# Kernel tuning notes

Hardware: AMD Instinct MI355X
Metric: run time of the kernel (lower is better)

Reference implementation:

```python
import jax, jax.numpy as jnp
import numpy as np

N_NODES = 100000
N_EDGES = 1600000
IN_FEATS = 64
OUT_FEATS = 16
NUM_HEADS = 4
EDGE_DIM = 5
NEG_SLOPE = 0.2


def setup_inputs() -> dict:
    key = jax.random.key(0)
    ks = jax.random.split(key, 16)
    H, D, Ed, Fi = NUM_HEADS, OUT_FEATS, EDGE_DIM, IN_FEATS
    inp = {
        "feat": jax.random.normal(ks[0], (N_NODES, Fi), jnp.float32),
        "edge_fea": jax.random.normal(ks[1], (N_EDGES, Ed), jnp.float32),
        "src": jax.random.randint(ks[2], (N_EDGES,), 0, N_NODES, jnp.int32),
        "dst": jax.random.randint(ks[3], (N_EDGES,), 0, N_NODES, jnp.int32),
        # params (xavier-ish scaling)
        "W_fc": jax.random.normal(ks[4], (Fi, H * D), jnp.float32) * (2.0 / np.sqrt(Fi + H * D)),
        "W_edg": jax.random.normal(ks[5], (Ed, H * Ed), jnp.float32) * (2.0 / np.sqrt(Ed + H * Ed)),
        "b_edg": jnp.zeros((H * Ed,), jnp.float32),
        "attn_l": jax.random.normal(ks[6], (H, D), jnp.float32) * 0.1,
        "attn_r": jax.random.normal(ks[7], (H, D), jnp.float32) * 0.1,
        "attn_edg": jax.random.normal(ks[8], (H, Ed), jnp.float32) * 0.1,
        "W_out": jax.random.normal(ks[9], (Ed + D, D), jnp.float32) * (2.0 / np.sqrt(Ed + 2 * D)),
        "b_out": jnp.zeros((D,), jnp.float32),
        "bias": jnp.zeros((H * D,), jnp.float32),
    }
    return inp


def reference(feat, edge_fea, src, dst, W_fc, W_edg, b_edg,
              attn_l, attn_r, attn_edg, W_out, b_out, bias):
    N = feat.shape[0]
    H, D = attn_l.shape
    Ed = attn_edg.shape[1]

    # node / edge projections
    feat_p = (feat @ W_fc).reshape(N, H, D)                 # [N,H,D]
    edge_p = (edge_fea @ W_edg + b_edg).reshape(-1, H, Ed)  # [E,H,Ed]

    # per-head attention logits
    el = jnp.einsum('nhd,hd->nh', feat_p, attn_l)           # [N,H]
    er = jnp.einsum('nhd,hd->nh', feat_p, attn_r)           # [N,H]
    ee = jnp.einsum('ehd,hd->eh', edge_p, attn_edg)         # [E,H]
    e = el[src] + er[dst] + ee                              # u_add_v + edge term
    e = jnp.where(e > 0, e, NEG_SLOPE * e)                  # leaky relu

    # edge softmax grouped by destination node
    m = jax.ops.segment_max(e, dst, num_segments=N)         # [N,H]
    a = jnp.exp(e - m[dst])
    z = jax.ops.segment_sum(a, dst, num_segments=N)
    a = a / z[dst]                                          # [E,H]

    # two scatter-aggregate passes
    ft_f = jax.ops.segment_sum(a[:, :, None] * edge_p, dst, num_segments=N)        # [N,H,Ed]
    ft = jax.ops.segment_sum(a[:, :, None] * feat_p[src], dst, num_segments=N)     # [N,H,D]

    rst = jnp.concatenate([ft_f, ft], axis=-1) @ W_out + b_out  # [N,H,D]
    rst = rst + bias.reshape(1, H, D)
    return rst
```

## Files before the change

kernel.cpp:

```cpp
#include <hip/hip_runtime.h>
#include <hip/hip_bf16.h>
#include <math.h>

#define NHEADS 4
#define DOUT 16
#define EDIM 5
#define CAP 128

__global__ __launch_bounds__(256) void node_proj_kernel(
    const float* __restrict__ feat, const float* __restrict__ W_fc,
    const float* __restrict__ attn_l, const float* __restrict__ attn_r,
    float* __restrict__ feat_p, float* __restrict__ el_er, int N) {
  __shared__ float wfc[64 * 64];
  for (int i = threadIdx.x; i < 64 * 64; i += 256) wfc[i] = W_fc[i];
  __syncthreads();
  const int wid  = threadIdx.x >> 6;
  const int lane = threadIdx.x & 63;
  const int n = blockIdx.x * 4 + wid;
  if (n >= N) return;

  const float f = feat[(size_t)n * 64 + lane];
  float acc = 0.f;
#pragma unroll
  for (int k = 0; k < 64; ++k) {
    const float fk = __shfl(f, k);
    acc += fk * wfc[k * 64 + lane];
  }
  feat_p[(size_t)n * 64 + lane] = acc;

  float al = acc * attn_l[lane];
  float ar = acc * attn_r[lane];
#pragma unroll
  for (int off = 1; off < 16; off <<= 1) {
    al += __shfl_xor(al, off);
    ar += __shfl_xor(ar, off);
  }
  if ((lane & 15) == 0) {
    const int h = lane >> 4;
    el_er[(size_t)n * 8 + h]     = al;
    el_er[(size_t)n * 8 + 4 + h] = ar;
  }
}

__global__ __launch_bounds__(256) void edge_logits_hist_kernel(
    const float* __restrict__ edge_fea, const int* __restrict__ src,
    const int* __restrict__ dst, const float* __restrict__ el_er,
    const float* __restrict__ W_edg, const float* __restrict__ b_edg,
    const float* __restrict__ attn_edg, float* __restrict__ e_logits,
    int* __restrict__ deg, int* __restrict__ rank, int E) {
  const int e = blockIdx.x * blockDim.x + threadIdx.x;
  if (e >= E) return;
  const int s = src[e];
  const int d = dst[e];
  rank[e] = atomicAdd(&deg[d], 1);

  float ef[5];
#pragma unroll
  for (int k = 0; k < 5; ++k) ef[k] = edge_fea[(size_t)e * 5 + k];

  const float4 elv = *(const float4*)(el_er + (size_t)s * 8);
  const float4 erv = *(const float4*)(el_er + (size_t)d * 8 + 4);
  const float elh[4] = {elv.x, elv.y, elv.z, elv.w};
  const float erh[4] = {erv.x, erv.y, erv.z, erv.w};

  float out[4];
#pragma unroll
  for (int h = 0; h < 4; ++h) {
    float ee = 0.f;
#pragma unroll
    for (int ed = 0; ed < 5; ++ed) {
      float ep = b_edg[h * 5 + ed];
#pragma unroll
      for (int k = 0; k < 5; ++k) ep += ef[k] * W_edg[k * 20 + h * 5 + ed];
      ee += ep * attn_edg[h * 5 + ed];
    }
    const float lg = elh[h] + erh[h] + ee;
    out[h] = (lg > 0.f) ? lg : 0.2f * lg;
  }
  *(float4*)(e_logits + (size_t)e * 4) = make_float4(out[0], out[1], out[2], out[3]);
}

__global__ __launch_bounds__(256) void scan_reduce_kernel(
    const int* __restrict__ deg, int* __restrict__ partial, int N) {
  const int base = blockIdx.x * 1024;
  int sum = 0;
  for (int i = threadIdx.x; i < 1024; i += 256) {
    const int idx = base + i;
    sum += (idx < N) ? deg[idx] : 0;
  }
#pragma unroll
  for (int off = 32; off >= 1; off >>= 1) sum += __shfl_xor(sum, off);
  __shared__ int ws[4];
  if ((threadIdx.x & 63) == 0) ws[threadIdx.x >> 6] = sum;
  __syncthreads();
  if (threadIdx.x == 0) partial[blockIdx.x] = ws[0] + ws[1] + ws[2] + ws[3];
}

__global__ __launch_bounds__(256) void scan_partials_kernel(
    int* __restrict__ partial, int nb) {
  __shared__ int buf[256];
  __shared__ int carry_s;
  const int t = threadIdx.x;
  if (t == 0) carry_s = 0;
  __syncthreads();
  for (int base = 0; base < nb; base += 256) {
    const int i = base + t;
    const int v = (i < nb) ? partial[i] : 0;
    buf[t] = v;
    __syncthreads();
    for (int off = 1; off < 256; off <<= 1) {
      const int tmp = (t >= off) ? buf[t - off] : 0;
      __syncthreads();
      buf[t] += tmp;
      __syncthreads();
    }
    const int carry = carry_s;
    if (i < nb) partial[i] = carry + buf[t] - v;
    __syncthreads();
    if (t == 255) carry_s = carry + buf[255];
    __syncthreads();
  }
}

__global__ __launch_bounds__(256) void scan_final_kernel(
    const int* __restrict__ deg, const int* __restrict__ partial,
    int* __restrict__ row_off, int N, int E) {
  const int b = blockIdx.x;
  const int t = threadIdx.x;
  const int lane = t & 63;
  const int wid = t >> 6;
  const int base = b * 1024 + t * 4;
  int v[4];
#pragma unroll
  for (int q = 0; q < 4; ++q) {
    const int idx = base + q;
    v[q] = (idx < N) ? deg[idx] : 0;
  }
  const int tsum = v[0] + v[1] + v[2] + v[3];
  int x = tsum;
#pragma unroll
  for (int off = 1; off < 64; off <<= 1) {
    const int tt = __shfl_up(x, off);
    if (lane >= off) x += tt;
  }
  __shared__ int ws[4];
  if (lane == 63) ws[wid] = x;
  __syncthreads();
  int wbase = 0;
  for (int w = 0; w < wid; ++w) wbase += ws[w];
  int run = partial[b] + wbase + (x - tsum);
#pragma unroll
  for (int q = 0; q < 4; ++q) {
    const int idx = base + q;
    if (idx < N) row_off[idx] = run;
    run += v[q];
  }
  if (b == 0 && t == 0) row_off[N] = E;
}

__global__ __launch_bounds__(256) void scatter_kernel(
    const int* __restrict__ dst, const int* __restrict__ row_off,
    const int* __restrict__ rank, int* __restrict__ perm, int E) {
  const int e = blockIdx.x * blockDim.x + threadIdx.x;
  if (e >= E) return;
  perm[row_off[dst[e]] + rank[e]] = e;
}

__global__ __launch_bounds__(256) void aggregate_kernel(
    const float* __restrict__ feat_p, const float* __restrict__ e_logits,
    const float* __restrict__ edge_fea, const int* __restrict__ src,
    const int* __restrict__ row_off, const int* __restrict__ perm,
    const float* __restrict__ W_edg, const float* __restrict__ b_edg,
    const float* __restrict__ W_out, const float* __restrict__ b_out,
    const float* __restrict__ bias, float* __restrict__ out, int N) {
  __shared__ float p_lds[4][CAP * 4];
  __shared__ int   s_lds[4][CAP];
  __shared__ float ef_lds[4][5 * CAP];

  const int wave = threadIdx.x >> 6;
  const int lane = threadIdx.x & 63;
  const int n = blockIdx.x * 4 + wave;
  if (n >= N) return;
  const int h = lane >> 4;
  const int d = lane & 15;

  float wcol[5];
  float be = 0.f;
  if (d < 5) {
    be = b_edg[h * 5 + d];
#pragma unroll
    for (int k = 0; k < 5; ++k) wcol[k] = W_edg[k * 20 + h * 5 + d];
  }

  const int beg = row_off[n];
  const int end = row_off[n + 1];
  const int deg = end - beg;

  float ft = 0.f, ftf = 0.f;

  if (deg <= CAP) {
    float4 mx = make_float4(-INFINITY, -INFINITY, -INFINITY, -INFINITY);
    for (int j0 = 0; j0 < deg; j0 += 64) {
      const int j = j0 + lane;
      if (j < deg) {
        const int e = perm[beg + j];
        const float4 lg = *(const float4*)(e_logits + (size_t)e * 4);
        s_lds[wave][j] = src[e];
        *(float4*)&p_lds[wave][j * 4] = lg;
#pragma unroll
        for (int k = 0; k < 5; ++k)
          ef_lds[wave][k * CAP + j] = edge_fea[(size_t)e * 5 + k];
        mx.x = fmaxf(mx.x, lg.x);
        mx.y = fmaxf(mx.y, lg.y);
        mx.z = fmaxf(mx.z, lg.z);
        mx.w = fmaxf(mx.w, lg.w);
      }
    }
#pragma unroll
    for (int off = 32; off >= 1; off >>= 1) {
      mx.x = fmaxf(mx.x, __shfl_xor(mx.x, off));
      mx.y = fmaxf(mx.y, __shfl_xor(mx.y, off));
      mx.z = fmaxf(mx.z, __shfl_xor(mx.z, off));
      mx.w = fmaxf(mx.w, __shfl_xor(mx.w, off));
    }

    float4 z = make_float4(0.f, 0.f, 0.f, 0.f);
    float4 wef[5];
#pragma unroll
    for (int k = 0; k < 5; ++k) wef[k] = make_float4(0.f, 0.f, 0.f, 0.f);
    for (int j0 = 0; j0 < deg; j0 += 64) {
      const int j = j0 + lane;
      if (j < deg) {
        const float4 lg = *(const float4*)&p_lds[wave][j * 4];
        float4 p;
        p.x = __expf(lg.x - mx.x);
        p.y = __expf(lg.y - mx.y);
        p.z = __expf(lg.z - mx.z);
        p.w = __expf(lg.w - mx.w);
        *(float4*)&p_lds[wave][j * 4] = p;
        z.x += p.x; z.y += p.y; z.z += p.z; z.w += p.w;
#pragma unroll
        for (int k = 0; k < 5; ++k) {
          const float efk = ef_lds[wave][k * CAP + j];
          wef[k].x += p.x * efk;
          wef[k].y += p.y * efk;
          wef[k].z += p.z * efk;
          wef[k].w += p.w * efk;
        }
      }
    }
#pragma unroll
    for (int off = 32; off >= 1; off >>= 1) {
      z.x += __shfl_xor(z.x, off);
      z.y += __shfl_xor(z.y, off);
      z.z += __shfl_xor(z.z, off);
      z.w += __shfl_xor(z.w, off);
#pragma unroll
      for (int k = 0; k < 5; ++k) {
        wef[k].x += __shfl_xor(wef[k].x, off);
        wef[k].y += __shfl_xor(wef[k].y, off);
        wef[k].z += __shfl_xor(wef[k].z, off);
        wef[k].w += __shfl_xor(wef[k].w, off);
      }
    }

    int j = 0;
    for (; j + 4 <= deg; j += 4) {
      const float p0 = p_lds[wave][(j + 0) * 4 + h];
      const float p1 = p_lds[wave][(j + 1) * 4 + h];
      const float p2 = p_lds[wave][(j + 2) * 4 + h];
      const float p3 = p_lds[wave][(j + 3) * 4 + h];
      const int s0 = s_lds[wave][j + 0];
      const int s1 = s_lds[wave][j + 1];
      const int s2 = s_lds[wave][j + 2];
      const int s3 = s_lds[wave][j + 3];
      const float f0 = feat_p[(size_t)s0 * 64 + lane];
      const float f1 = feat_p[(size_t)s1 * 64 + lane];
      const float f2 = feat_p[(size_t)s2 * 64 + lane];
      const float f3 = feat_p[(size_t)s3 * 64 + lane];
      ft += p0 * f0 + p1 * f1 + p2 * f2 + p3 * f3;
    }
    for (; j < deg; ++j) {
      const float p = p_lds[wave][j * 4 + h];
      const int s = s_lds[wave][j];
      ft += p * feat_p[(size_t)s * 64 + lane];
    }

    const float zh = (h == 0) ? z.x : (h == 1) ? z.y : (h == 2) ? z.z : z.w;
    const float inv = (zh > 0.f) ? 1.f / zh : 0.f;
    ft *= inv;
    if (d < 5) {
      float acc = 0.f;
#pragma unroll
      for (int k = 0; k < 5; ++k) {
        const float wk = (h == 0) ? wef[k].x : (h == 1) ? wef[k].y
                        : (h == 2) ? wef[k].z : wef[k].w;
        acc += wk * wcol[k];
      }
      ftf = acc * inv + ((zh > 0.f) ? be : 0.f);
    }
  } else {
    float mx0 = -INFINITY, mx1 = -INFINITY, mx2 = -INFINITY, mx3 = -INFINITY;
    for (int i = beg + lane; i < end; i += 64) {
      const int e = perm[i];
      const float4 lg = *(const float4*)(e_logits + (size_t)e * 4);
      mx0 = fmaxf(mx0, lg.x);
      mx1 = fmaxf(mx1, lg.y);
      mx2 = fmaxf(mx2, lg.z);
      mx3 = fmaxf(mx3, lg.w);
    }
#pragma unroll
    for (int off = 32; off >= 1; off >>= 1) {
      mx0 = fmaxf(mx0, __shfl_xor(mx0, off));
      mx1 = fmaxf(mx1, __shfl_xor(mx1, off));
      mx2 = fmaxf(mx2, __shfl_xor(mx2, off));
      mx3 = fmaxf(mx3, __shfl_xor(mx3, off));
    }
    const float mh = (h == 0) ? mx0 : (h == 1) ? mx1 : (h == 2) ? mx2 : mx3;
    float z = 0.f;
    for (int i = beg; i < end; ++i) {
      const int e = perm[i];
      const int s = src[e];
      const float lg = e_logits[(size_t)e * 4 + h];
      const float p = __expf(lg - mh);
      z += p;
      ft += p * feat_p[(size_t)s * 64 + lane];
      if (d < 5) {
        float ep = be;
#pragma unroll
        for (int k = 0; k < 5; ++k) ep += edge_fea[(size_t)e * 5 + k] * wcol[k];
        ftf += p * ep;
      }
    }
    const float inv = (z > 0.f) ? 1.f / z : 0.f;
    ft *= inv;
    ftf *= inv;
  }

  float acc = b_out[d] + bias[lane];
#pragma unroll
  for (int k = 0; k < 5; ++k)
    acc += __shfl(ftf, h * 16 + k) * W_out[k * 16 + d];
#pragma unroll
  for (int k = 0; k < 16; ++k)
    acc += __shfl(ft, h * 16 + k) * W_out[(5 + k) * 16 + d];

  out[(size_t)n * 64 + lane] = acc;
}

extern "C" void kernel_launch(void* const* d_in, const int* in_sizes, int n_in,
                              void* d_out, int out_size, void* d_ws, size_t ws_size,
                              hipStream_t stream) {
  const float* feat     = (const float*)d_in[0];
  const float* edge_fea = (const float*)d_in[1];
  const int*   src      = (const int*)d_in[2];
  const int*   dst      = (const int*)d_in[3];
  const float* W_fc     = (const float*)d_in[4];
  const float* W_edg    = (const float*)d_in[5];
  const float* b_edg    = (const float*)d_in[6];
  const float* attn_l   = (const float*)d_in[7];
  const float* attn_r   = (const float*)d_in[8];
  const float* attn_edg = (const float*)d_in[9];
  const float* W_out    = (const float*)d_in[10];
  const float* b_out    = (const float*)d_in[11];
  const float* bias     = (const float*)d_in[12];

  const int N = in_sizes[0] / 64;
  const int E = in_sizes[2];
  float* out = (float*)d_out;

  char* ws = (char*)d_ws;
  size_t off = 0;
  auto alloc = [&](size_t bytes) -> void* {
    void* p = ws + off;
    off = (off + bytes + 255) & ~(size_t)255;
    return p;
  };
  float* feat_p   = (float*)alloc((size_t)N * 64 * 4);
  float* el_er    = (float*)alloc((size_t)N * 8 * 4);
  float* e_logits = (float*)alloc((size_t)E * 4 * 4);
  int*   deg      = (int*)alloc((size_t)N * 4);
  int*   rank     = (int*)alloc((size_t)E * 4);
  int*   row_off  = (int*)alloc((size_t)(N + 1) * 4);
  int*   perm     = (int*)alloc((size_t)E * 4);
  int*   partial  = (int*)alloc((size_t)1024 * 4);
  (void)ws_size; (void)n_in; (void)out_size;

  hipMemsetAsync(deg, 0, (size_t)N * 4, stream);

  const int nblk_nodes = (N + 3) / 4;
  const int nblk_edges = (E + 255) / 256;
  const int nb_scan = (N + 1023) / 1024;

  node_proj_kernel<<<nblk_nodes, 256, 0, stream>>>(feat, W_fc, attn_l, attn_r,
                                                   feat_p, el_er, N);
  edge_logits_hist_kernel<<<nblk_edges, 256, 0, stream>>>(
      edge_fea, src, dst, el_er, W_edg, b_edg, attn_edg, e_logits, deg, rank, E);
  scan_reduce_kernel<<<nb_scan, 256, 0, stream>>>(deg, partial, N);
  scan_partials_kernel<<<1, 256, 0, stream>>>(partial, nb_scan);
  scan_final_kernel<<<nb_scan, 256, 0, stream>>>(deg, partial, row_off, N, E);
  scatter_kernel<<<nblk_edges, 256, 0, stream>>>(dst, row_off, rank, perm, E);
  aggregate_kernel<<<nblk_nodes, 256, 0, stream>>>(
      feat_p, e_logits, edge_fea, src, row_off, perm, W_edg, b_edg, W_out,
      b_out, bias, out, N);
}
```

Baseline: 536.0 us.

## Fuse edge-logit computation into aggregation and scatter edge data into CSR order

```diff
diff --git a/kernel.cpp b/kernel.cpp
--- a/kernel.cpp
+++ b/kernel.cpp
@@ -42,42 +42,12 @@
   }
 }
 
-__global__ __launch_bounds__(256) void edge_logits_hist_kernel(
-    const float* __restrict__ edge_fea, const int* __restrict__ src,
-    const int* __restrict__ dst, const float* __restrict__ el_er,
-    const float* __restrict__ W_edg, const float* __restrict__ b_edg,
-    const float* __restrict__ attn_edg, float* __restrict__ e_logits,
-    int* __restrict__ deg, int* __restrict__ rank, int E) {
+__global__ __launch_bounds__(256) void rank_kernel(
+    const int* __restrict__ dst, int* __restrict__ deg,
+    int* __restrict__ rank, int E) {
   const int e = blockIdx.x * blockDim.x + threadIdx.x;
   if (e >= E) return;
-  const int s = src[e];
-  const int d = dst[e];
-  rank[e] = atomicAdd(&deg[d], 1);
-
-  float ef[5];
-#pragma unroll
-  for (int k = 0; k < 5; ++k) ef[k] = edge_fea[(size_t)e * 5 + k];
-
-  const float4 elv = *(const float4*)(el_er + (size_t)s * 8);
-  const float4 erv = *(const float4*)(el_er + (size_t)d * 8 + 4);
-  const float elh[4] = {elv.x, elv.y, elv.z, elv.w};
-  const float erh[4] = {erv.x, erv.y, erv.z, erv.w};
-
-  float out[4];
-#pragma unroll
-  for (int h = 0; h < 4; ++h) {
-    float ee = 0.f;
-#pragma unroll
-    for (int ed = 0; ed < 5; ++ed) {
-      float ep = b_edg[h * 5 + ed];
-#pragma unroll
-      for (int k = 0; k < 5; ++k) ep += ef[k] * W_edg[k * 20 + h * 5 + ed];
-      ee += ep * attn_edg[h * 5 + ed];
-    }
-    const float lg = elh[h] + erh[h] + ee;
-    out[h] = (lg > 0.f) ? lg : 0.2f * lg;
-  }
-  *(float4*)(e_logits + (size_t)e * 4) = make_float4(out[0], out[1], out[2], out[3]);
+  rank[e] = atomicAdd(&deg[dst[e]], 1);
 }
 
 __global__ __launch_bounds__(256) void scan_reduce_kernel(
@@ -159,23 +129,29 @@
 }
 
 __global__ __launch_bounds__(256) void scatter_kernel(
-    const int* __restrict__ dst, const int* __restrict__ row_off,
-    const int* __restrict__ rank, int* __restrict__ perm, int E) {
+    const int* __restrict__ dst, const int* __restrict__ src,
+    const float* __restrict__ edge_fea, const int* __restrict__ row_off,
+    const int* __restrict__ rank, int* __restrict__ src_csr,
+    float* __restrict__ ef_csr, int E) {
   const int e = blockIdx.x * blockDim.x + threadIdx.x;
   if (e >= E) return;
-  perm[row_off[dst[e]] + rank[e]] = e;
+  const int pos = row_off[dst[e]] + rank[e];
+  src_csr[pos] = src[e];
+#pragma unroll
+  for (int k = 0; k < 5; ++k)
+    ef_csr[(size_t)pos * 5 + k] = edge_fea[(size_t)e * 5 + k];
 }
 
 __global__ __launch_bounds__(256) void aggregate_kernel(
-    const float* __restrict__ feat_p, const float* __restrict__ e_logits,
-    const float* __restrict__ edge_fea, const int* __restrict__ src,
-    const int* __restrict__ row_off, const int* __restrict__ perm,
+    const float* __restrict__ feat_p, const float* __restrict__ el_er,
+    const int* __restrict__ src_csr, const float* __restrict__ ef_csr,
+    const int* __restrict__ row_off,
     const float* __restrict__ W_edg, const float* __restrict__ b_edg,
+    const float* __restrict__ attn_edg,
     const float* __restrict__ W_out, const float* __restrict__ b_out,
     const float* __restrict__ bias, float* __restrict__ out, int N) {
   __shared__ float p_lds[4][CAP * 4];
   __shared__ int   s_lds[4][CAP];
-  __shared__ float ef_lds[4][5 * CAP];
 
   const int wave = threadIdx.x >> 6;
   const int lane = threadIdx.x & 63;
@@ -184,6 +160,24 @@
   const int h = lane >> 4;
   const int d = lane & 15;
 
+  float g[5][4];
+  float c0[4];
+#pragma unroll
+  for (int hh = 0; hh < 4; ++hh) {
+    float c = 0.f;
+#pragma unroll
+    for (int ed = 0; ed < 5; ++ed) c += b_edg[hh * 5 + ed] * attn_edg[hh * 5 + ed];
+    c0[hh] = c;
+#pragma unroll
+    for (int k = 0; k < 5; ++k) {
+      float s = 0.f;
+#pragma unroll
+      for (int ed = 0; ed < 5; ++ed)
+        s += W_edg[k * 20 + hh * 5 + ed] * attn_edg[hh * 5 + ed];
+      g[k][hh] = s;
+    }
+  }
+
   float wcol[5];
   float be = 0.f;
   if (d < 5) {
@@ -192,6 +186,7 @@
     for (int k = 0; k < 5; ++k) wcol[k] = W_edg[k * 20 + h * 5 + d];
   }
 
+  const float4 er4 = *(const float4*)(el_er + (size_t)n * 8 + 4);
   const int beg = row_off[n];
   const int end = row_off[n + 1];
   const int deg = end - beg;
@@ -199,31 +194,6 @@
   float ft = 0.f, ftf = 0.f;
 
   if (deg <= CAP) {
-    float4 mx = make_float4(-INFINITY, -INFINITY, -INFINITY, -INFINITY);
-    for (int j0 = 0; j0 < deg; j0 += 64) {
-      const int j = j0 + lane;
-      if (j < deg) {
-        const int e = perm[beg + j];
-        const float4 lg = *(const float4*)(e_logits + (size_t)e * 4);
-        s_lds[wave][j] = src[e];
-        *(float4*)&p_lds[wave][j * 4] = lg;
-#pragma unroll
-        for (int k = 0; k < 5; ++k)
-          ef_lds[wave][k * CAP + j] = edge_fea[(size_t)e * 5 + k];
-        mx.x = fmaxf(mx.x, lg.x);
-        mx.y = fmaxf(mx.y, lg.y);
-        mx.z = fmaxf(mx.z, lg.z);
-        mx.w = fmaxf(mx.w, lg.w);
-      }
-    }
-#pragma unroll
-    for (int off = 32; off >= 1; off >>= 1) {
-      mx.x = fmaxf(mx.x, __shfl_xor(mx.x, off));
-      mx.y = fmaxf(mx.y, __shfl_xor(mx.y, off));
-      mx.z = fmaxf(mx.z, __shfl_xor(mx.z, off));
-      mx.w = fmaxf(mx.w, __shfl_xor(mx.w, off));
-    }
-
     float4 z = make_float4(0.f, 0.f, 0.f, 0.f);
     float4 wef[5];
 #pragma unroll
@@ -231,21 +201,33 @@
     for (int j0 = 0; j0 < deg; j0 += 64) {
       const int j = j0 + lane;
       if (j < deg) {
-        const float4 lg = *(const float4*)&p_lds[wave][j * 4];
+        const int i = beg + j;
+        const int s = src_csr[i];
+        float ef[5];
+#pragma unroll
+        for (int k = 0; k < 5; ++k) ef[k] = ef_csr[(size_t)i * 5 + k];
+        const float4 el4 = *(const float4*)(el_er + (size_t)s * 8);
+        float lgh[4] = {el4.x + er4.x + c0[0], el4.y + er4.y + c0[1],
+                        el4.z + er4.z + c0[2], el4.w + er4.w + c0[3]};
+#pragma unroll
+        for (int k = 0; k < 5; ++k) {
+#pragma unroll
+          for (int hh = 0; hh < 4; ++hh) lgh[hh] += ef[k] * g[k][hh];
+        }
         float4 p;
-        p.x = __expf(lg.x - mx.x);
-        p.y = __expf(lg.y - mx.y);
-        p.z = __expf(lg.z - mx.z);
-        p.w = __expf(lg.w - mx.w);
+        p.x = __expf(lgh[0] > 0.f ? lgh[0] : 0.2f * lgh[0]);
+        p.y = __expf(lgh[1] > 0.f ? lgh[1] : 0.2f * lgh[1]);
+        p.z = __expf(lgh[2] > 0.f ? lgh[2] : 0.2f * lgh[2]);
+        p.w = __expf(lgh[3] > 0.f ? lgh[3] : 0.2f * lgh[3]);
+        s_lds[wave][j] = s;
         *(float4*)&p_lds[wave][j * 4] = p;
         z.x += p.x; z.y += p.y; z.z += p.z; z.w += p.w;
 #pragma unroll
         for (int k = 0; k < 5; ++k) {
-          const float efk = ef_lds[wave][k * CAP + j];
-          wef[k].x += p.x * efk;
-          wef[k].y += p.y * efk;
-          wef[k].z += p.z * efk;
-          wef[k].w += p.w * efk;
+          wef[k].x += p.x * ef[k];
+          wef[k].y += p.y * ef[k];
+          wef[k].z += p.z * ef[k];
+          wef[k].w += p.w * ef[k];
         }
       }
     }
@@ -300,41 +282,31 @@
       ftf = acc * inv + ((zh > 0.f) ? be : 0.f);
     }
   } else {
-    float mx0 = -INFINITY, mx1 = -INFINITY, mx2 = -INFINITY, mx3 = -INFINITY;
-    for (int i = beg + lane; i < end; i += 64) {
-      const int e = perm[i];
-      const float4 lg = *(const float4*)(e_logits + (size_t)e * 4);
-      mx0 = fmaxf(mx0, lg.x);
-      mx1 = fmaxf(mx1, lg.y);
-      mx2 = fmaxf(mx2, lg.z);
-      mx3 = fmaxf(mx3, lg.w);
-    }
-#pragma unroll
-    for (int off = 32; off >= 1; off >>= 1) {
-      mx0 = fmaxf(mx0, __shfl_xor(mx0, off));
-      mx1 = fmaxf(mx1, __shfl_xor(mx1, off));
-      mx2 = fmaxf(mx2, __shfl_xor(mx2, off));
-      mx3 = fmaxf(mx3, __shfl_xor(mx3, off));
-    }
-    const float mh = (h == 0) ? mx0 : (h == 1) ? mx1 : (h == 2) ? mx2 : mx3;
     float z = 0.f;
+    float wefh[5] = {0.f, 0.f, 0.f, 0.f, 0.f};
+    const float erh = (h == 0) ? er4.x : (h == 1) ? er4.y : (h == 2) ? er4.z : er4.w;
     for (int i = beg; i < end; ++i) {
-      const int e = perm[i];
-      const int s = src[e];
-      const float lg = e_logits[(size_t)e * 4 + h];
-      const float p = __expf(lg - mh);
+      const int s = src_csr[i];
+      float ef[5];
+#pragma unroll
+      for (int k = 0; k < 5; ++k) ef[k] = ef_csr[(size_t)i * 5 + k];
+      float lg = el_er[(size_t)s * 8 + h] + erh + c0[h];
+#pragma unroll
+      for (int k = 0; k < 5; ++k) lg += ef[k] * g[k][h];
+      const float p = __expf(lg > 0.f ? lg : 0.2f * lg);
       z += p;
       ft += p * feat_p[(size_t)s * 64 + lane];
-      if (d < 5) {
-        float ep = be;
-#pragma unroll
-        for (int k = 0; k < 5; ++k) ep += edge_fea[(size_t)e * 5 + k] * wcol[k];
-        ftf += p * ep;
-      }
+#pragma unroll
+      for (int k = 0; k < 5; ++k) wefh[k] += p * ef[k];
     }
     const float inv = (z > 0.f) ? 1.f / z : 0.f;
     ft *= inv;
-    ftf *= inv;
+    if (d < 5) {
+      float acc = 0.f;
+#pragma unroll
+      for (int k = 0; k < 5; ++k) acc += wefh[k] * wcol[k];
+      ftf = acc * inv + ((z > 0.f) ? be : 0.f);
+    }
   }
 
   float acc = b_out[d] + bias[lane];
@@ -376,14 +348,14 @@
     off = (off + bytes + 255) & ~(size_t)255;
     return p;
   };
-  float* feat_p   = (float*)alloc((size_t)N * 64 * 4);
-  float* el_er    = (float*)alloc((size_t)N * 8 * 4);
-  float* e_logits = (float*)alloc((size_t)E * 4 * 4);
-  int*   deg      = (int*)alloc((size_t)N * 4);
-  int*   rank     = (int*)alloc((size_t)E * 4);
-  int*   row_off  = (int*)alloc((size_t)(N + 1) * 4);
-  int*   perm     = (int*)alloc((size_t)E * 4);
-  int*   partial  = (int*)alloc((size_t)1024 * 4);
+  float* feat_p  = (float*)alloc((size_t)N * 64 * 4);
+  float* el_er   = (float*)alloc((size_t)N * 8 * 4);
+  int*   deg     = (int*)alloc((size_t)N * 4);
+  int*   rank    = (int*)alloc((size_t)E * 4);
+  int*   row_off = (int*)alloc((size_t)(N + 1) * 4);
+  int*   src_csr = (int*)alloc((size_t)E * 4);
+  float* ef_csr  = (float*)alloc((size_t)E * 5 * 4);
+  int*   partial = (int*)alloc((size_t)1024 * 4);
   (void)ws_size; (void)n_in; (void)out_size;
 
   hipMemsetAsync(deg, 0, (size_t)N * 4, stream);
@@ -394,13 +366,13 @@
 
   node_proj_kernel<<<nblk_nodes, 256, 0, stream>>>(feat, W_fc, attn_l, attn_r,
                                                    feat_p, el_er, N);
-  edge_logits_hist_kernel<<<nblk_edges, 256, 0, stream>>>(
-      edge_fea, src, dst, el_er, W_edg, b_edg, attn_edg, e_logits, deg, rank, E);
+  rank_kernel<<<nblk_edges, 256, 0, stream>>>(dst, deg, rank, E);
   scan_reduce_kernel<<<nb_scan, 256, 0, stream>>>(deg, partial, N);
   scan_partials_kernel<<<1, 256, 0, stream>>>(partial, nb_scan);
   scan_final_kernel<<<nb_scan, 256, 0, stream>>>(deg, partial, row_off, N, E);
-  scatter_kernel<<<nblk_edges, 256, 0, stream>>>(dst, row_off, rank, perm, E);
+  scatter_kernel<<<nblk_edges, 256, 0, stream>>>(dst, src, edge_fea, row_off,
+                                                 rank, src_csr, ef_csr, E);
   aggregate_kernel<<<nblk_nodes, 256, 0, stream>>>(
-      feat_p, e_logits, edge_fea, src, row_off, perm, W_edg, b_edg, W_out,
+      feat_p, el_er, src_csr, ef_csr, row_off, W_edg, b_edg, attn_edg, W_out,
       b_out, bias, out, N);
 }
```

Result: slower. 605.8 us (+13.0%).
